# Optimization experiments

Hardware: AMD Instinct MI355X
Metric: run time of the kernel (lower is better)

## Reference

```python
import jax, jax.numpy as jnp
import numpy as np

B, T, L = 32, 800, 60
H = 512           # decoder hidden
D = 2 * H         # encoder feature dim (bidirectional)
A = 512           # attention hidden
FC = 16           # attention conv filters
K = 101           # attention conv kernel (odd -> SAME padding)
C = 4000          # num classes


def setup_inputs() -> dict:
    key = jax.random.key(0)
    ks = jax.random.split(key, 20)
    sc = lambda n: 1.0 / np.sqrt(n)
    inp = {
        "hbatch": jax.random.normal(ks[0], (B, T, D), jnp.float32),
        "lengths": jnp.sort(jax.random.randint(ks[1], (B,), 1, T + 1)),
        "targets": jax.random.uniform(ks[2], (B, L, C), jnp.float32),
        # decoder weights
        "W_sy": jax.random.normal(ks[3], (H, H), jnp.float32) * sc(H),
        "W_gy": jax.random.normal(ks[4], (H, D), jnp.float32) * sc(D),
        "b_gy": jnp.zeros((H,), jnp.float32),
        "W_yy": jax.random.normal(ks[5], (C, H), jnp.float32) * sc(H),
        "b_yy": jnp.zeros((C,), jnp.float32),
        "W_ys": jax.random.normal(ks[6], (4 * H, C), jnp.float32) * sc(C),
        "W_ss": jax.random.normal(ks[7], (4 * H, H), jnp.float32) * sc(H),
        "W_gs": jax.random.normal(ks[8], (4 * H, D), jnp.float32) * sc(D),
        "b_gs": jnp.zeros((4 * H,), jnp.float32),
        # location-aware attention weights
        "W_se": jax.random.normal(ks[9], (A, H), jnp.float32) * sc(H),
        "W_he": jax.random.normal(ks[10], (A, D), jnp.float32) * sc(D),
        "W_fe": jax.random.normal(ks[11], (A, FC), jnp.float32) * sc(FC),
        "conv_w": jax.random.normal(ks[12], (FC, 1, K), jnp.float32) * sc(K),
        "conv_b": jnp.zeros((FC,), jnp.float32),
        "w_ee": jax.random.normal(ks[13], (A,), jnp.float32) * sc(A),
    }
    return inp


def _sig(x):  # tanh-based sigmoid used by the custom LSTM cell (== sigmoid)
    return jnp.tanh(x * 0.5) * 0.5 + 0.5


def _decode(hbatch, targets, lengths, W_sy, W_gy, b_gy, W_yy, b_yy,
            W_ys, W_ss, W_gs, b_gs, W_se, W_he, W_fe, conv_w, conv_b, w_ee):
    mask = jnp.arange(T)[None, :] < lengths[:, None]          # [B,T]
    hE = jnp.einsum('btd,ad->bta', hbatch, W_he)              # precomputed enc proj
    t_seq = jnp.swapaxes(targets, 0, 1)                       # [L,B,C]

    def conv_feat(alpha):                                     # alpha [B,T]
        y = jax.lax.conv_general_dilated(
            alpha[:, None, :], conv_w, (1,), 'SAME',
            dimension_numbers=('NCH', 'OIH', 'NCH'))          # [B,FC,T]
        y = y + conv_b[None, :, None]
        return jnp.einsum('bft,af->bta', y, W_fe)             # [B,T,A]

    def step(carry, t_step):
        s, c, alpha = carry
        sE = s @ W_se.T                                       # [B,A]
        e = jnp.tanh(sE[:, None, :] + hE + conv_feat(alpha)) @ w_ee  # [B,T]
        e = jnp.where(mask, e, -1e30)
        alpha = jax.nn.softmax(e, axis=1)
        g = jnp.einsum('bt,btd->bd', alpha, hbatch)           # [B,D]
        y = jnp.tanh(g @ W_gy.T + b_gy + s @ W_sy.T) @ W_yy.T + b_yy
        rec = t_step @ W_ys.T + s @ W_ss.T + g @ W_gs.T + b_gs
        i, f, cg, o = jnp.split(rec, 4, axis=1)
        c = _sig(f) * c + _sig(i) * jnp.tanh(cg)
        s = _sig(o) * jnp.tanh(c)
        return (s, c, alpha), y

    init = (jnp.zeros((B, H), hbatch.dtype), jnp.zeros((B, H), hbatch.dtype),
            jnp.zeros((B, T), hbatch.dtype))
    _, ys = jax.lax.scan(step, init, t_seq)                   # [L,B,C]
    return jnp.swapaxes(ys, 0, 1)                             # [B,L,C]


def reference(hbatch, lengths, targets, W_sy, W_gy, b_gy, W_yy, b_yy,
              W_ys, W_ss, W_gs, b_gs, W_se, W_he, W_fe, conv_w, conv_b, w_ee):
    return _decode(hbatch, targets, lengths, W_sy, W_gy, b_gy, W_yy, b_yy,
                   W_ys, W_ss, W_gs, b_gs, W_se, W_he, W_fe, conv_w, conv_b, w_ee)
```

## Files before the change

### kernel.cpp

```cpp
#include <hip/hip_runtime.h>
#include <hip/hip_bf16.h>
#include <math.h>

#define B_  32
#define T_  800
#define L_  60
#define H_  512
#define D_  1024
#define A_  512
#define FC_ 16
#define K_  101
#define C_  4000
#define TT_ 64
#define KC_ 1536
#define NB_ 512

typedef short bf16x8 __attribute__((ext_vector_type(8)));
typedef float f32x4 __attribute__((ext_vector_type(4)));

__device__ __forceinline__ float fast_tanh(float x) {
  x = fminf(15.f, fmaxf(-15.f, x));
  float e = __expf(2.f * x);
  return (e - 1.f) / (e + 1.f);
}
__device__ __forceinline__ float fast_sig(float x) {
  return 1.f / (1.f + __expf(-x));
}
__device__ __forceinline__ float bflo(unsigned int u) {
  union { unsigned int i; float f; } v; v.i = u << 16; return v.f;
}
__device__ __forceinline__ float bfhi(unsigned int u) {
  union { unsigned int i; float f; } v; v.i = u & 0xffff0000u; return v.f;
}
__device__ __forceinline__ unsigned short f2bf(float f) {
  union { float f; unsigned int i; } v; v.f = f;
  unsigned int r = v.i + 0x7fff + ((v.i >> 16) & 1);
  return (unsigned short)(r >> 16);
}

__device__ __forceinline__ float cload(const float* p2) {
  return __hip_atomic_load(p2, __ATOMIC_RELAXED, __HIP_MEMORY_SCOPE_AGENT);
}
__device__ __forceinline__ void cstore(float* p2, float v) {
  __hip_atomic_store(p2, v, __ATOMIC_RELAXED, __HIP_MEMORY_SCOPE_AGENT);
}

__device__ __forceinline__ void grid_barrier(unsigned int* bar, int nb,
                                             unsigned int ep) {
  __syncthreads();
  if (threadIdx.x == 0) {
    asm volatile("s_waitcnt vmcnt(0)" ::: "memory");
    const int g = blockIdx.x & 15;
    const unsigned int gsz = (unsigned int)(nb >> 4);
    unsigned int old = __hip_atomic_fetch_add(&bar[g * 32], 1u,
                                              __ATOMIC_RELAXED,
                                              __HIP_MEMORY_SCOPE_AGENT);
    if (old == ep * gsz - 1u) {
      unsigned int ro = __hip_atomic_fetch_add(&bar[512], 1u,
                                               __ATOMIC_RELAXED,
                                               __HIP_MEMORY_SCOPE_AGENT);
      if (ro == ep * 16u - 1u) {
#pragma unroll
        for (int i = 0; i < 16; i++)
          __hip_atomic_store(&bar[544 + i * 32], ep, __ATOMIC_RELAXED,
                             __HIP_MEMORY_SCOPE_AGENT);
      }
    }
    while (__hip_atomic_load(&bar[544 + g * 32], __ATOMIC_RELAXED,
                             __HIP_MEMORY_SCOPE_AGENT) < ep) {
      __builtin_amdgcn_s_sleep(4);
    }
  }
  asm volatile("" ::: "memory");
  __syncthreads();
}

__global__ __launch_bounds__(256) void gemm_bf16_nt(
    const unsigned short* __restrict__ Am, const unsigned short* __restrict__ Bm,
    float* __restrict__ O, unsigned short* __restrict__ Obf,
    const float* __restrict__ bias, int M, int N, int K)
{
  __shared__ unsigned short sA[128 * 40];
  __shared__ unsigned short sB[128 * 40];
  const int tid = threadIdx.x;
  const int mt = blockIdx.y * 128, nt = blockIdx.x * 128;
  const int wave = tid >> 6, lane = tid & 63;
  const int wm = (wave & 1) * 64, wn = (wave >> 1) * 64;
  const int qd = lane >> 4, md = lane & 15;

  f32x4 acc[4][4];
#pragma unroll
  for (int i = 0; i < 4; i++)
#pragma unroll
    for (int j = 0; j < 4; j++) acc[i][j] = (f32x4){0.f, 0.f, 0.f, 0.f};

  for (int k0 = 0; k0 < K; k0 += 32) {
#pragma unroll
    for (int p = 0; p < 2; p++) {
      int idx = tid + p * 256;
      int r = idx >> 2, kq = (idx & 3) * 8;
      *(uint4*)&sA[r * 40 + kq] =
          *(const uint4*)&Am[(size_t)(mt + r) * K + k0 + kq];
      uint4 bv = make_uint4(0, 0, 0, 0);
      if (nt + r < N) bv = *(const uint4*)&Bm[(size_t)(nt + r) * K + k0 + kq];
      *(uint4*)&sB[r * 40 + kq] = bv;
    }
    __syncthreads();
    bf16x8 af[4], bfr[4];
#pragma unroll
    for (int i = 0; i < 4; i++) {
      af[i]  = *(const bf16x8*)&sA[(wm + i * 16 + md) * 40 + qd * 8];
      bfr[i] = *(const bf16x8*)&sB[(wn + i * 16 + md) * 40 + qd * 8];
    }
#pragma unroll
    for (int mi = 0; mi < 4; mi++)
#pragma unroll
      for (int ni = 0; ni < 4; ni++)
        acc[mi][ni] = __builtin_amdgcn_mfma_f32_16x16x32_bf16(
            af[mi], bfr[ni], acc[mi][ni], 0, 0, 0);
    __syncthreads();
  }

#pragma unroll
  for (int mi = 0; mi < 4; mi++)
#pragma unroll
    for (int ni = 0; ni < 4; ni++) {
      int gn = nt + wn + ni * 16 + md;
      if (gn >= N) continue;
      float bv = bias ? bias[gn] : 0.f;
#pragma unroll
      for (int reg = 0; reg < 4; reg++) {
        int gm = mt + wm + mi * 16 + qd * 4 + reg;
        float v = acc[mi][ni][reg] + bv;
        if (Obf) Obf[(size_t)gm * N + gn] = f2bf(v);
        else     O[(size_t)gm * N + gn] = v;
      }
    }
}

__global__ __launch_bounds__(256) void k_cvt_f4(
    const float4* __restrict__ in, ushort4* __restrict__ out, int n4)
{
  int i = blockIdx.x * 256 + threadIdx.x;
  if (i < n4) {
    float4 v = in[i];
    ushort4 o;
    o.x = f2bf(v.x); o.y = f2bf(v.y); o.z = f2bf(v.z); o.w = f2bf(v.w);
    out[i] = o;
  }
}

__global__ __launch_bounds__(256) void k_build_wcell(
    const float* __restrict__ W_gy, const float* __restrict__ W_sy,
    const float* __restrict__ W_gs, const float* __restrict__ W_ss,
    unsigned short* __restrict__ Wc)
{
  int idx = blockIdx.x * 256 + threadIdx.x;
  if (idx >= 5 * H_ * KC_) return;
  int row = idx / KC_;
  int k = idx - row * KC_;
  int gt = row >> 9, h = row & (H_ - 1);
  float v;
  if (gt == 0)
    v = (k < D_) ? W_gy[(size_t)h * D_ + k] : W_sy[(size_t)h * H_ + (k - D_)];
  else {
    int r = (gt - 1) * H_ + h;
    v = (k < D_) ? W_gs[(size_t)r * D_ + k] : W_ss[(size_t)r * H_ + (k - D_)];
  }
  Wc[idx] = f2bf(v);
}

struct DecP {
  const unsigned short* hEbf;
  const unsigned short* hbbf;
  const unsigned short* Wcell;
  const unsigned short* W_sebf;
  const float* TY;
  const float* conv_w;
  const float* conv_b;
  const float* W_fe;
  const float* w_ee;
  const float* b_gy;
  const float* b_gs;
  const int* lengths;
  float* alpha;
  float* e;
  float* g;
  float* part;
  float* s0;
  float* s1;
  float* c;
  float* sE;
  unsigned short* u_all;
  unsigned int* bar;
  int nb;
};

__global__ __launch_bounds__(256) void k_decode(DecP p)
{
  const int bid = blockIdx.x;
  const int tid = threadIdx.x;
  const int nb = p.nb;

  __shared__ float s_wfeT[FC_ * A_];
  __shared__ float s_cw[FC_ * K_];
  __shared__ float s_wee[A_];
  __shared__ float s_alpha[TT_ + K_ - 1];
  __shared__ float s_cf[TT_ * FC_];
  __shared__ float s_sE[A_];
  __shared__ float redA[256];
  __shared__ float redB[256];
  __shared__ float a_sh[256];
  __shared__ float sx[32 * 193];
  __shared__ float sv[H_];

  for (int idx = tid; idx < FC_ * A_; idx += 256) {
    int f = idx >> 9, a = idx & (A_ - 1);
    s_wfeT[idx] = p.W_fe[a * FC_ + f];
  }
  for (int idx = tid; idx < FC_ * K_; idx += 256) s_cw[idx] = p.conv_w[idx];
  for (int idx = tid; idx < A_; idx += 256) s_wee[idx] = p.w_ee[idx];

  float* s_in = p.s0;
  float* s_out = p.s1;
  unsigned int ep = 0;

  for (int l = 0; l < L_; l++) {
    for (int tile = bid; tile < 13 * B_; tile += nb) {
      const int b = tile / 13;
      const int t0 = (tile - b * 13) * TT_;
      const int len = p.lengths[b];
      if (t0 >= len) continue;
      for (int idx = tid; idx < TT_ + K_ - 1; idx += 256) {
        int t = t0 - (K_ / 2) + idx;
        s_alpha[idx] = (t >= 0 && t < T_) ? cload(&p.alpha[b * T_ + t]) : 0.f;
      }
      for (int idx = tid; idx < A_; idx += 256)
        s_sE[idx] = cload(&p.sE[b * A_ + idx]);
      __syncthreads();

      for (int idx = tid; idx < TT_ * FC_; idx += 256) {
        int tl = idx >> 4, f = idx & 15;
        float acc2 = p.conv_b[f];
        for (int k = 0; k < K_; k++)
          acc2 = fmaf(s_alpha[tl + k], s_cw[f * K_ + k], acc2);
        s_cf[tl * FC_ + f] = acc2;
      }
      __syncthreads();

      const int wave = tid >> 6, lane = tid & 63;
      for (int tl = wave; tl < TT_; tl += 4) {
        int t = t0 + tl;
        if (t >= len) continue;
        float cf[FC_];
#pragma unroll
        for (int f = 0; f < FC_; f++) cf[f] = s_cf[tl * FC_ + f];
        const unsigned short* hEp = p.hEbf + ((size_t)(b * T_ + t)) * A_;
        float pt = 0.f;
#pragma unroll
        for (int j = 0; j < 4; j++) {
          int a0 = j * 128 + lane * 2;
          float F0 = 0.f, F1 = 0.f;
#pragma unroll
          for (int f = 0; f < FC_; f++) {
            float2 wf = *(const float2*)&s_wfeT[f * A_ + a0];
            F0 = fmaf(wf.x, cf[f], F0);
            F1 = fmaf(wf.y, cf[f], F1);
          }
          unsigned int hp = *(const unsigned int*)&hEp[a0];
          float v0 = fast_tanh(s_sE[a0] + bflo(hp) + F0);
          float v1 = fast_tanh(s_sE[a0 + 1] + bfhi(hp) + F1);
          pt = fmaf(s_wee[a0], v0, pt);
          pt = fmaf(s_wee[a0 + 1], v1, pt);
        }
#pragma unroll
        for (int off = 32; off > 0; off >>= 1) pt += __shfl_down(pt, off);
        if (lane == 0) cstore(&p.e[b * T_ + t], pt);
      }
      __syncthreads();
    }
    grid_barrier(p.bar, nb, ++ep);

    for (int u = bid; u < 512; u += nb) {
      const int b = u & 31;
      const int d0 = (u >> 5) * 64;
      const int len = p.lengths[b];
      for (int t = tid; t < len; t += 256) s_cf[t] = cload(&p.e[b * T_ + t]);
      __syncthreads();
      float m = -3.0e38f;
      for (int t = tid; t < len; t += 256) m = fmaxf(m, s_cf[t]);
      redA[tid] = m;
      __syncthreads();
      for (int s2 = 128; s2 > 0; s2 >>= 1) {
        if (tid < s2) redA[tid] = fmaxf(redA[tid], redA[tid + s2]);
        __syncthreads();
      }
      m = redA[0];
      __syncthreads();
      float zs = 0.f;
      for (int t = tid; t < len; t += 256) zs += __expf(s_cf[t] - m);
      redA[tid] = zs;
      __syncthreads();
      for (int s2 = 128; s2 > 0; s2 >>= 1) {
        if (tid < s2) redA[tid] += redA[tid + s2];
        __syncthreads();
      }
      const float invZ = 1.f / redA[0];
      __syncthreads();

      const int dloc = (tid & 31) * 2, tph = tid >> 5;
      float g0 = 0.f, g1 = 0.f;
      for (int tb = 0; tb < len; tb += 256) {
        int t = tb + tid;
        float av = (t < len) ? __expf(s_cf[t] - m) * invZ : 0.f;
        a_sh[tid] = av;
        __syncthreads();
        if (d0 == 0 && t < len) cstore(&p.alpha[b * T_ + t], av);
        int cnt = min(256, len - tb);
        for (int tt = tph; tt < cnt; tt += 8) {
          unsigned int hp = *(const unsigned int*)
              &p.hbbf[((size_t)(b * T_ + tb + tt)) * D_ + d0 + dloc];
          float av2 = a_sh[tt];
          g0 = fmaf(av2, bflo(hp), g0);
          g1 = fmaf(av2, bfhi(hp), g1);
        }
        __syncthreads();
      }
      redA[tid] = g0;
      redB[tid] = g1;
      __syncthreads();
      if (tid < 32) {
        float r0 = 0.f, r1 = 0.f;
#pragma unroll
        for (int k2 = 0; k2 < 8; k2++) {
          r0 += redA[tid + 32 * k2];
          r1 += redB[tid + 32 * k2];
        }
        cstore(&p.g[b * D_ + d0 + 2 * tid],     r0);
        cstore(&p.g[b * D_ + d0 + 2 * tid + 1], r1);
      }
      __syncthreads();
    }
    grid_barrier(p.bar, nb, ++ep);

    for (int u = bid; u < 512; u += nb) {
      const int ks = u >> 6;
      const int xb = u & 63;
      const int k0 = ks * 192;
      for (int i = tid; i < 32 * 192; i += 256) {
        int bb = i / 192, dd = i - bb * 192;
        int k = k0 + dd;
        sx[bb * 193 + dd] = (k < D_) ? cload(&p.g[bb * D_ + k])
                                     : cload(&s_in[bb * H_ + (k - D_)]);
      }
      __syncthreads();
      const int gid = xb * 256 + tid;
      const int b = gid & 31, h = gid >> 5;
      const float* xp = &sx[b * 193];
      float acc[5] = {0.f, 0.f, 0.f, 0.f, 0.f};
      const uint4* w[5];
#pragma unroll
      for (int gt = 0; gt < 5; gt++)
        w[gt] = (const uint4*)(p.Wcell + ((size_t)(gt * H_ + h)) * KC_ + k0);
#pragma unroll 4
      for (int i = 0; i < 24; i++) {
        uint4 uu[5];
#pragma unroll
        for (int gt = 0; gt < 5; gt++) uu[gt] = w[gt][i];
        float xv[8];
#pragma unroll
        for (int e2 = 0; e2 < 8; e2++) xv[e2] = xp[i * 8 + e2];
#pragma unroll
        for (int gt = 0; gt < 5; gt++) {
          acc[gt] = fmaf(bflo(uu[gt].x), xv[0], acc[gt]);
          acc[gt] = fmaf(bfhi(uu[gt].x), xv[1], acc[gt]);
          acc[gt] = fmaf(bflo(uu[gt].y), xv[2], acc[gt]);
          acc[gt] = fmaf(bfhi(uu[gt].y), xv[3], acc[gt]);
          acc[gt] = fmaf(bflo(uu[gt].z), xv[4], acc[gt]);
          acc[gt] = fmaf(bfhi(uu[gt].z), xv[5], acc[gt]);
          acc[gt] = fmaf(bflo(uu[gt].w), xv[6], acc[gt]);
          acc[gt] = fmaf(bfhi(uu[gt].w), xv[7], acc[gt]);
        }
      }
#pragma unroll
      for (int gt = 0; gt < 5; gt++)
        cstore(&p.part[(size_t)(ks * 5 + gt) * 16384 + b * 512 + h], acc[gt]);
      __syncthreads();
    }
    grid_barrier(p.bar, nb, ++ep);

    if (bid < 32) {
      const int b = bid;
      const float* ty = p.TY + ((size_t)b * L_ + l) * (4 * H_);
      for (int h = tid; h < H_; h += 256) {
        float s5[5] = {0.f, 0.f, 0.f, 0.f, 0.f};
#pragma unroll
        for (int ks = 0; ks < 8; ks++)
#pragma unroll
          for (int gt = 0; gt < 5; gt++)
            s5[gt] += cload(&p.part[(size_t)(ks * 5 + gt) * 16384 + b * 512 + h]);
        float uv = fast_tanh(s5[0] + p.b_gy[h]);
        float iv = s5[1] + ty[h] + p.b_gs[h];
        float fv = s5[2] + ty[h + H_] + p.b_gs[h + H_];
        float cg2 = s5[3] + ty[h + 2 * H_] + p.b_gs[h + 2 * H_];
        float ov = s5[4] + ty[h + 3 * H_] + p.b_gs[h + 3 * H_];
        float cn = fast_sig(fv) * p.c[b * H_ + h] + fast_sig(iv) * fast_tanh(cg2);
        p.c[b * H_ + h] = cn;
        float sn = fast_sig(ov) * fast_tanh(cn);
        cstore(&s_out[b * H_ + h], sn);
        sv[h] = sn;
        p.u_all[((size_t)b * L_ + l) * H_ + h] = f2bf(uv);
      }
      __syncthreads();
      for (int a = tid; a < A_; a += 256) {
        const uint4* row = (const uint4*)(p.W_sebf + (size_t)a * H_);
        float acc = 0.f;
#pragma unroll 8
        for (int i = 0; i < 64; i++) {
          uint4 ww = row[i];
          const float* xp2 = &sv[i * 8];
          acc = fmaf(bflo(ww.x), xp2[0], acc);
          acc = fmaf(bfhi(ww.x), xp2[1], acc);
          acc = fmaf(bflo(ww.y), xp2[2], acc);
          acc = fmaf(bfhi(ww.y), xp2[3], acc);
          acc = fmaf(bflo(ww.z), xp2[4], acc);
          acc = fmaf(bfhi(ww.z), xp2[5], acc);
          acc = fmaf(bflo(ww.w), xp2[6], acc);
          acc = fmaf(bfhi(ww.w), xp2[7], acc);
        }
        cstore(&p.sE[b * A_ + a], acc);
      }
    }
    grid_barrier(p.bar, nb, ++ep);

    float* tmp = s_in; s_in = s_out; s_out = tmp;
  }
}

extern "C" void kernel_launch(void* const* d_in, const int* in_sizes, int n_in,
                              void* d_out, int out_size, void* d_ws, size_t ws_size,
                              hipStream_t stream)
{
  const float* hbatch  = (const float*)d_in[0];
  const int*   lengths = (const int*)d_in[1];
  const float* targets = (const float*)d_in[2];
  const float* W_sy = (const float*)d_in[3];
  const float* W_gy = (const float*)d_in[4];
  const float* b_gy = (const float*)d_in[5];
  const float* W_yy = (const float*)d_in[6];
  const float* b_yy = (const float*)d_in[7];
  const float* W_ys = (const float*)d_in[8];
  const float* W_ss = (const float*)d_in[9];
  const float* W_gs = (const float*)d_in[10];
  const float* b_gs = (const float*)d_in[11];
  const float* W_se = (const float*)d_in[12];
  const float* W_he = (const float*)d_in[13];
  const float* W_fe = (const float*)d_in[14];
  const float* conv_w = (const float*)d_in[15];
  const float* conv_b = (const float*)d_in[16];
  const float* w_ee   = (const float*)d_in[17];
  float* out = (float*)d_out;

  char* ws = (char*)d_ws;
  size_t off = 0;
  auto alloc = [&](size_t bytes) -> void* {
    void* p = ws + off;
    off += (bytes + 255) & ~(size_t)255;
    return p;
  };
  unsigned short* hEbf   = (unsigned short*)alloc((size_t)B_ * T_ * A_ * 2);
  unsigned short* hbbf   = (unsigned short*)alloc((size_t)B_ * T_ * D_ * 2);
  unsigned short* Wcell  = (unsigned short*)alloc((size_t)5 * H_ * KC_ * 2);
  unsigned short* Wyybf  = (unsigned short*)alloc((size_t)C_ * H_ * 2);
  unsigned short* W_hebf = (unsigned short*)alloc((size_t)A_ * D_ * 2);
  unsigned short* W_sebf = (unsigned short*)alloc((size_t)A_ * H_ * 2);
  unsigned short* u_all  = (unsigned short*)alloc((size_t)B_ * L_ * H_ * 2);
  float* TY    = (float*)alloc((size_t)B_ * L_ * 4 * H_ * 4);
  float* part  = (float*)alloc((size_t)8 * 5 * 16384 * 4);
  float* alpha = (float*)alloc((size_t)B_ * T_ * 4);
  float* e     = (float*)alloc((size_t)B_ * T_ * 4);
  float* g     = (float*)alloc((size_t)B_ * D_ * 4);
  float* s0    = (float*)alloc((size_t)B_ * H_ * 4);
  float* s1    = (float*)alloc((size_t)B_ * H_ * 4);
  float* c     = (float*)alloc((size_t)B_ * H_ * 4);
  float* sE    = (float*)alloc((size_t)B_ * A_ * 4);
  unsigned int* bar = (unsigned int*)alloc(8192);

  unsigned short* targetsbf = hEbf;
  unsigned short* W_ysbf    = hbbf;

  (void)hipMemsetAsync(alpha, 0, (size_t)B_ * T_ * 4, stream);
  (void)hipMemsetAsync(s0, 0, (size_t)B_ * H_ * 4, stream);
  (void)hipMemsetAsync(c, 0, (size_t)B_ * H_ * 4, stream);
  (void)hipMemsetAsync(sE, 0, (size_t)B_ * A_ * 4, stream);
  (void)hipMemsetAsync(bar, 0, 8192, stream);

  {
    int n4t = B_ * L_ * C_ / 4;
    k_cvt_f4<<<(n4t + 255) / 256, 256, 0, stream>>>((const float4*)targets,
                                                    (ushort4*)targetsbf, n4t);
    int n4w = 4 * H_ * C_ / 4;
    k_cvt_f4<<<(n4w + 255) / 256, 256, 0, stream>>>((const float4*)W_ys,
                                                    (ushort4*)W_ysbf, n4w);
    gemm_bf16_nt<<<dim3(2048 / 128, 1920 / 128), 256, 0, stream>>>(
        targetsbf, W_ysbf, TY, nullptr, nullptr, 1920, 2048, 4000);

    int n4h = B_ * T_ * D_ / 4;
    k_cvt_f4<<<(n4h + 255) / 256, 256, 0, stream>>>((const float4*)hbatch,
                                                    (ushort4*)hbbf, n4h);
    int n4e = A_ * D_ / 4;
    k_cvt_f4<<<(n4e + 255) / 256, 256, 0, stream>>>((const float4*)W_he,
                                                    (ushort4*)W_hebf, n4e);
    gemm_bf16_nt<<<dim3(A_ / 128, (B_ * T_) / 128), 256, 0, stream>>>(
        hbbf, W_hebf, nullptr, hEbf, nullptr, B_ * T_, A_, D_);

    int n4y = C_ * H_ / 4;
    k_cvt_f4<<<(n4y + 255) / 256, 256, 0, stream>>>((const float4*)W_yy,
                                                    (ushort4*)Wyybf, n4y);
    int n4s = A_ * H_ / 4;
    k_cvt_f4<<<(n4s + 255) / 256, 256, 0, stream>>>((const float4*)W_se,
                                                    (ushort4*)W_sebf, n4s);
    int nw = 5 * H_ * KC_;
    k_build_wcell<<<(nw + 255) / 256, 256, 0, stream>>>(W_gy, W_sy, W_gs, W_ss,
                                                        Wcell);
  }

  DecP p;
  p.hEbf = hEbf; p.hbbf = hbbf; p.Wcell = Wcell; p.W_sebf = W_sebf;
  p.TY = TY; p.conv_w = conv_w; p.conv_b = conv_b; p.W_fe = W_fe;
  p.w_ee = w_ee; p.b_gy = b_gy; p.b_gs = b_gs; p.lengths = lengths;
  p.alpha = alpha; p.e = e; p.g = g; p.part = part;
  p.s0 = s0; p.s1 = s1; p.c = c; p.sE = sE; p.u_all = u_all;
  p.bar = bar; p.nb = NB_;
  k_decode<<<dim3(NB_), dim3(256), 0, stream>>>(p);

  gemm_bf16_nt<<<dim3((C_ + 127) / 128, 1920 / 128), 256, 0, stream>>>(
      u_all, Wyybf, out, nullptr, b_yy, 1920, C_, H_);
}
```

Measured before the change: 6.706 ms.

## Map attention tiles one-per-block, prefetch hE loads, and warm L2 from idle blocks

```diff
diff --git a/kernel.cpp b/kernel.cpp
--- a/kernel.cpp
+++ b/kernel.cpp
@@ -11,7 +11,7 @@
 #define FC_ 16
 #define K_  101
 #define C_  4000
-#define TT_ 64
+#define TT_ 50
 #define KC_ 1536
 #define NB_ 512
 
@@ -68,7 +68,7 @@
     }
     while (__hip_atomic_load(&bar[544 + g * 32], __ATOMIC_RELAXED,
                              __HIP_MEMORY_SCOPE_AGENT) < ep) {
-      __builtin_amdgcn_s_sleep(4);
+      __builtin_amdgcn_s_sleep(2);
     }
   }
   asm volatile("" ::: "memory");
@@ -206,7 +206,7 @@
   __shared__ float s_cw[FC_ * K_];
   __shared__ float s_wee[A_];
   __shared__ float s_alpha[TT_ + K_ - 1];
-  __shared__ float s_cf[TT_ * FC_];
+  __shared__ float s_cf[800];
   __shared__ float s_sE[A_];
   __shared__ float redA[256];
   __shared__ float redB[256];
@@ -226,58 +226,64 @@
   unsigned int ep = 0;
 
   for (int l = 0; l < L_; l++) {
-    for (int tile = bid; tile < 13 * B_; tile += nb) {
-      const int b = tile / 13;
-      const int t0 = (tile - b * 13) * TT_;
+    {
+      const int tile = bid;
+      const int b = tile >> 4;
+      const int t0 = (tile & 15) * TT_;
       const int len = p.lengths[b];
-      if (t0 >= len) continue;
-      for (int idx = tid; idx < TT_ + K_ - 1; idx += 256) {
-        int t = t0 - (K_ / 2) + idx;
-        s_alpha[idx] = (t >= 0 && t < T_) ? cload(&p.alpha[b * T_ + t]) : 0.f;
-      }
-      for (int idx = tid; idx < A_; idx += 256)
-        s_sE[idx] = cload(&p.sE[b * A_ + idx]);
-      __syncthreads();
-
-      for (int idx = tid; idx < TT_ * FC_; idx += 256) {
-        int tl = idx >> 4, f = idx & 15;
-        float acc2 = p.conv_b[f];
-        for (int k = 0; k < K_; k++)
-          acc2 = fmaf(s_alpha[tl + k], s_cw[f * K_ + k], acc2);
-        s_cf[tl * FC_ + f] = acc2;
-      }
-      __syncthreads();
-
-      const int wave = tid >> 6, lane = tid & 63;
-      for (int tl = wave; tl < TT_; tl += 4) {
-        int t = t0 + tl;
-        if (t >= len) continue;
-        float cf[FC_];
-#pragma unroll
-        for (int f = 0; f < FC_; f++) cf[f] = s_cf[tl * FC_ + f];
-        const unsigned short* hEp = p.hEbf + ((size_t)(b * T_ + t)) * A_;
-        float pt = 0.f;
-#pragma unroll
-        for (int j = 0; j < 4; j++) {
-          int a0 = j * 128 + lane * 2;
-          float F0 = 0.f, F1 = 0.f;
-#pragma unroll
-          for (int f = 0; f < FC_; f++) {
-            float2 wf = *(const float2*)&s_wfeT[f * A_ + a0];
-            F0 = fmaf(wf.x, cf[f], F0);
-            F1 = fmaf(wf.y, cf[f], F1);
+      if (t0 < len) {
+        for (int idx = tid; idx < TT_ + K_ - 1; idx += 256) {
+          int t = t0 - (K_ / 2) + idx;
+          s_alpha[idx] = (t >= 0 && t < T_) ? cload(&p.alpha[b * T_ + t]) : 0.f;
+        }
+        for (int idx = tid; idx < A_; idx += 256)
+          s_sE[idx] = cload(&p.sE[b * A_ + idx]);
+        __syncthreads();
+
+        for (int idx = tid; idx < TT_ * FC_; idx += 256) {
+          int tl = idx >> 4, f = idx & 15;
+          float acc2 = p.conv_b[f];
+          for (int k = 0; k < K_; k++)
+            acc2 = fmaf(s_alpha[tl + k], s_cw[f * K_ + k], acc2);
+          s_cf[tl * FC_ + f] = acc2;
+        }
+        __syncthreads();
+
+        const int wave = tid >> 6, lane = tid & 63;
+        for (int tl = wave; tl < TT_; tl += 4) {
+          int t = t0 + tl;
+          if (t >= len) continue;
+          float cf[FC_];
+#pragma unroll
+          for (int f = 0; f < FC_; f++) cf[f] = s_cf[tl * FC_ + f];
+          const unsigned short* hEp = p.hEbf + ((size_t)(b * T_ + t)) * A_;
+          unsigned int hp0 = *(const unsigned int*)&hEp[0 * 128 + lane * 2];
+          unsigned int hp1 = *(const unsigned int*)&hEp[1 * 128 + lane * 2];
+          unsigned int hp2 = *(const unsigned int*)&hEp[2 * 128 + lane * 2];
+          unsigned int hp3 = *(const unsigned int*)&hEp[3 * 128 + lane * 2];
+          unsigned int hps[4] = {hp0, hp1, hp2, hp3};
+          float pt = 0.f;
+#pragma unroll
+          for (int j = 0; j < 4; j++) {
+            int a0 = j * 128 + lane * 2;
+            float F0 = 0.f, F1 = 0.f;
+#pragma unroll
+            for (int f = 0; f < FC_; f++) {
+              float2 wf = *(const float2*)&s_wfeT[f * A_ + a0];
+              F0 = fmaf(wf.x, cf[f], F0);
+              F1 = fmaf(wf.y, cf[f], F1);
+            }
+            float v0 = fast_tanh(s_sE[a0] + bflo(hps[j]) + F0);
+            float v1 = fast_tanh(s_sE[a0 + 1] + bfhi(hps[j]) + F1);
+            pt = fmaf(s_wee[a0], v0, pt);
+            pt = fmaf(s_wee[a0 + 1], v1, pt);
           }
-          unsigned int hp = *(const unsigned int*)&hEp[a0];
-          float v0 = fast_tanh(s_sE[a0] + bflo(hp) + F0);
-          float v1 = fast_tanh(s_sE[a0 + 1] + bfhi(hp) + F1);
-          pt = fmaf(s_wee[a0], v0, pt);
-          pt = fmaf(s_wee[a0 + 1], v1, pt);
-        }
-#pragma unroll
-        for (int off = 32; off > 0; off >>= 1) pt += __shfl_down(pt, off);
-        if (lane == 0) cstore(&p.e[b * T_ + t], pt);
-      }
-      __syncthreads();
+#pragma unroll
+          for (int off = 32; off > 0; off >>= 1) pt += __shfl_down(pt, off);
+          if (lane == 0) cstore(&p.e[b * T_ + t], pt);
+        }
+        __syncthreads();
+      }
     }
     grid_barrier(p.bar, nb, ++ep);
 
@@ -310,6 +316,8 @@
 
       const int dloc = (tid & 31) * 2, tph = tid >> 5;
       float g0 = 0.f, g1 = 0.f;
+      const unsigned short* hbbase =
+          p.hbbf + (size_t)b * T_ * D_ + d0 + dloc;
       for (int tb = 0; tb < len; tb += 256) {
         int t = tb + tid;
         float av = (t < len) ? __expf(s_cf[t] - m) * invZ : 0.f;
@@ -317,12 +325,19 @@
         __syncthreads();
         if (d0 == 0 && t < len) cstore(&p.alpha[b * T_ + t], av);
         int cnt = min(256, len - tb);
-        for (int tt = tph; tt < cnt; tt += 8) {
-          unsigned int hp = *(const unsigned int*)
-              &p.hbbf[((size_t)(b * T_ + tb + tt)) * D_ + d0 + dloc];
+        int tt = tph;
+        unsigned int hpn = 0;
+        if (tt < cnt)
+          hpn = *(const unsigned int*)&hbbase[(size_t)(tb + tt) * D_];
+        while (tt < cnt) {
+          unsigned int hp = hpn;
+          int ttn = tt + 8;
+          if (ttn < cnt)
+            hpn = *(const unsigned int*)&hbbase[(size_t)(tb + ttn) * D_];
           float av2 = a_sh[tt];
           g0 = fmaf(av2, bflo(hp), g0);
           g1 = fmaf(av2, bfhi(hp), g1);
+          tt = ttn;
         }
         __syncthreads();
       }
@@ -429,6 +444,14 @@
           acc = fmaf(bfhi(ww.w), xp2[7], acc);
         }
         cstore(&p.sE[b * A_ + a], acc);
+      }
+    } else if (l + 1 < L_) {
+      const uint4* src = (const uint4*)p.hEbf;
+      const size_t n16 = (size_t)B_ * T_ * A_ * 2 / 16;
+      size_t i = (size_t)(bid - 32) * 256 + tid;
+      for (; i < n16; i += (size_t)480 * 256) {
+        uint4 v = src[i];
+        asm volatile("" :: "v"(v.x), "v"(v.y), "v"(v.z), "v"(v.w));
       }
     }
     grid_barrier(p.bar, nb, ++ep);
```

Result: no change. 6.606 ms (-1.5%).
